# Performance work log

Hardware: AMD Instinct MI355X
Metric: run time of the kernel (lower is better)

Reference implementation:

```python
import jax, jax.numpy as jnp
import numpy as np

B, T, D_MODEL, N_HEADS = 2, 2048, 2048, 16
D_HEAD = D_MODEL // N_HEADS
SCALE = 1.0 / np.sqrt(D_HEAD)


def setup_inputs() -> dict:
    key = jax.random.key(0)
    ks = jax.random.split(key, 5)
    w_std = 1.0 / np.sqrt(D_MODEL)
    x = jax.random.normal(ks[0], (B, T, D_MODEL), dtype=jnp.float32)
    W_q = jax.random.normal(ks[1], (D_MODEL, D_MODEL), dtype=jnp.float32) * w_std
    W_k = jax.random.normal(ks[2], (D_MODEL, D_MODEL), dtype=jnp.float32) * w_std
    W_v = jax.random.normal(ks[3], (D_MODEL, D_MODEL), dtype=jnp.float32) * w_std
    W_o = jax.random.normal(ks[4], (D_MODEL, D_MODEL), dtype=jnp.float32) * w_std
    return {"x": x, "W_q": W_q, "W_k": W_k, "W_v": W_v, "W_o": W_o}


def _split_heads(y):
    # [B, T, D] -> [B, H, T, d_head]
    b, t, _ = y.shape
    return y.reshape(b, t, N_HEADS, D_HEAD).transpose(0, 2, 1, 3)


def reference(x, W_q, W_k, W_v, W_o):
    # Linear layers (torch nn.Linear: y = x @ W.T)
    Q = _split_heads(x @ W_q.T)
    K = _split_heads(x @ W_k.T)
    V = _split_heads(x @ W_v.T)
    # Causal softmax attention (math-equivalent to the tiled online-softmax loop)
    scores = jnp.einsum('bhqd,bhkd->bhqk', Q, K) * SCALE
    causal_mask = jnp.tril(jnp.ones((T, T), dtype=bool))  # [T, T]
    scores = jnp.where(causal_mask, scores, -jnp.inf)
    P = jax.nn.softmax(scores, axis=-1)
    O = jnp.einsum('bhqk,bhkd->bhqd', P, V)
    out = O.transpose(0, 2, 1, 3).reshape(B, T, D_MODEL)  # merge heads
    return out @ W_o.T
```

## Files before the change

kernel.cpp:

```cpp
#include <hip/hip_runtime.h>
#include <hip/hip_bf16.h>
#include <hip/hip_fp16.h>

#define B_   2
#define T_   2048
#define DM   2048
#define NH   16
#define DH   128
#define M_   (B_*T_)
#define SCALE_ 0.08838834764831845f

typedef _Float16 f16;
typedef f16  half8 __attribute__((ext_vector_type(8)));
typedef f16  half4 __attribute__((ext_vector_type(4)));
typedef float f32x4 __attribute__((ext_vector_type(4)));

#define GL16(gp, lp) __builtin_amdgcn_global_load_lds( \
    (const __attribute__((address_space(1))) void*)(gp), \
    (__attribute__((address_space(3))) void*)(lp), 16, 0, 0)

#define MFMA16(a, b, c) __builtin_amdgcn_mfma_f32_16x16x32_f16((a), (b), (c), 0, 0, 0)

struct CvtArgs { const float* s[5]; f16* d[5]; };

__global__ __launch_bounds__(256) void convert_all(CvtArgs a) {
    size_t i4 = (size_t)blockIdx.x * 256 + threadIdx.x;
    int r; size_t off;
    if (i4 < 2097152) { r = 0; off = i4; }
    else { size_t k = i4 - 2097152; r = 1 + (int)(k >> 20); off = k & 1048575; }
    float4 v = *((const float4*)a.s[r] + off);
    half4 h;
    h[0] = (f16)v.x; h[1] = (f16)v.y; h[2] = (f16)v.z; h[3] = (f16)v.w;
    *((half4*)a.d[r] + off) = h;
}

#define NT_K 32

__global__ __launch_bounds__(512, 2)
void qkv3(const f16* __restrict__ A, const f16* __restrict__ Bw,
          f16* __restrict__ dst)
{
    __shared__ __align__(16) char smem[114688];

    const int tid  = threadIdx.x;
    const int lane = tid & 63;
    const int w    = tid >> 6;
    const int wr   = w >> 1, wc = w & 1;

    const int id = (blockIdx.x & 7) * 64 + (blockIdx.x >> 3);
    const int bm = id & 15, bn = id >> 4;
    const int m0 = bm * 256, n0 = bn * 192;

    const int scol8 = (((tid & 7) ^ ((tid >> 3) & 7)) << 3);
    const int rc0 = (((lane >> 4) * 16)      ) ^ ((lane & 7) << 4);
    const int rc1 = (64 + (lane >> 4) * 16   ) ^ ((lane & 7) << 4);

    f32x4 acc[4][6] = {};

#define QSTAGE_A(bufb, ch, s, kt) GL16( \
    A + (size_t)(m0 + (ch)*128 + (tid>>8)*64 + (s)*32 + ((tid>>3)&31)) * 2048 + (kt)*64 + scol8, \
    smem + (bufb)*57344 + (ch)*16384 + (s)*8192 + w*1024)
#define QSTAGE_B(bufb, u, kt) GL16( \
    Bw + (size_t)(n0 + (tid>>7)*48 + (u)*16 + ((tid>>3)&15)) * 2048 + (kt)*64 + scol8, \
    smem + (bufb)*57344 + 32768 + (u)*8192 + w*1024)

    const int abase = (wr >> 1) * 16384 + (wr & 1) * 4096 + (lane & 15) * 128;
    const int bbase = 32768 + wc * 4096 + (lane & 15) * 128;

    half8 af0[4][2], af1[4][2], bnx[2];

    QSTAGE_A(0, 0, 0, 0); QSTAGE_A(0, 0, 1, 0);
    QSTAGE_A(0, 1, 0, 0); QSTAGE_A(0, 1, 1, 0);
    QSTAGE_B(0, 0, 0);    QSTAGE_B(0, 1, 0);    QSTAGE_B(0, 2, 0);
    {
        asm volatile("s_waitcnt vmcnt(2)" ::: "memory");
        __builtin_amdgcn_s_barrier();
        __builtin_amdgcn_sched_barrier(0);
        const char* buf0 = smem;
        #pragma unroll
        for (int m = 0; m < 4; ++m) {
            const char* p = buf0 + (m >> 1) * 8192 + abase + (m & 1) * 2048;
            af0[m][0] = *(const half8*)(p + rc0);
            af0[m][1] = *(const half8*)(p + rc1);
        }
        bnx[0] = *(const half8*)(buf0 + bbase + rc0);
        bnx[1] = *(const half8*)(buf0 + bbase + rc1);
    }

#define GATE(n_) do { \
    asm volatile("s_waitcnt vmcnt(" #n_ ")" ::: "memory"); \
    __builtin_amdgcn_s_barrier(); \
    __builtin_amdgcn_sched_barrier(0); \
} while (0)

#define MFC(AF, BB, f_) do { \
    __builtin_amdgcn_s_setprio(1); \
    _Pragma("unroll") \
    for (int m_ = 0; m_ < 4; ++m_) { \
        acc[m_][f_] = MFMA16(AF[m_][0], (BB)[0], acc[m_][f_]); \
        acc[m_][f_] = MFMA16(AF[m_][1], (BB)[1], acc[m_][f_]); \
    } \
    __builtin_amdgcn_s_setprio(0); \
} while (0)

#define RDB(dstv, off) do { \
    const char* p_ = buf + bbase + (off); \
    dstv[0] = *(const half8*)(p_ + rc0); \
    dstv[1] = *(const half8*)(p_ + rc1); \
} while (0)

#define BODY(t_, c_, AFC, AFN) do { \
    const char* buf  = smem + (c_) * 57344; \
    const char* nbuf = smem + ((c_) ^ 1) * 57344; \
    const int  kt    = ((t_) + 1 < NT_K) ? (t_) + 1 : (t_); \
    half8 b3[2], b1[2], b4[2], b2[2], b5[2]; \
     \
    RDB(b3, 2048); \
    QSTAGE_A((c_) ^ 1, 0, 0, kt); QSTAGE_A((c_) ^ 1, 0, 1, kt); \
    MFC(AFC, bnx, 0); \
     \
    GATE(3); \
    RDB(b1, 8192); \
    QSTAGE_A((c_) ^ 1, 1, 0, kt); QSTAGE_A((c_) ^ 1, 1, 1, kt); \
    MFC(AFC, b3, 3); \
     \
    RDB(b4, 8192 + 2048); \
    QSTAGE_B((c_) ^ 1, 0, kt); \
    MFC(AFC, b1, 1); \
     \
    GATE(5); \
    RDB(b2, 16384); \
    QSTAGE_B((c_) ^ 1, 1, kt); \
    MFC(AFC, b4, 4); \
     \
    GATE(1); \
    RDB(b5, 16384 + 2048); \
    { const char* p_ = nbuf + abase; \
      AFN[0][0] = *(const half8*)(p_ + rc0); \
      AFN[0][1] = *(const half8*)(p_ + rc1); \
      AFN[1][0] = *(const half8*)(p_ + 2048 + rc0); \
      AFN[1][1] = *(const half8*)(p_ + 2048 + rc1); } \
    QSTAGE_B((c_) ^ 1, 2, kt); \
    MFC(AFC, b2, 2); \
     \
    { const char* p_ = nbuf + 8192 + abase; \
      AFN[2][0] = *(const half8*)(p_ + rc0); \
      AFN[2][1] = *(const half8*)(p_ + rc1); \
      AFN[3][0] = *(const half8*)(p_ + 2048 + rc0); \
      AFN[3][1] = *(const half8*)(p_ + 2048 + rc1); } \
    { const char* p_ = nbuf + bbase; \
      bnx[0] = *(const half8*)(p_ + rc0); \
      bnx[1] = *(const half8*)(p_ + rc1); } \
    MFC(AFC, b5, 5); \
} while (0)

    for (int t = 0; t < NT_K; t += 2) {
        BODY(t,     0, af0, af1);
        BODY(t + 1, 1, af1, af0);
    }
#undef BODY
#undef RDB
#undef MFC
#undef GATE
#undef QSTAGE_A
#undef QSTAGE_B

    asm volatile("s_waitcnt vmcnt(0)" ::: "memory");

    #pragma unroll
    for (int m = 0; m < 4; ++m)
        #pragma unroll
        for (int f = 0; f < 6; ++f)
            #pragma unroll
            for (int j = 0; j < 4; ++j) {
                int row  = m0 + wr * 64 + m * 16 + (lane >> 4) * 4 + j;
                int gcol = n0 + wc * 96 + f * 16 + (lane & 15);
                int sec = gcol >> 11, cic = gcol & 2047;
                int b = row >> 11, tt = row & (T_ - 1);
                int h = cic >> 7, d = cic & 127;
                float cs = (sec == 0) ? SCALE_ : 1.0f;
                dst[(size_t)sec * ((size_t)M_ * 2048) +
                    ((size_t)(b * NH + h) * T_ + tt) * DH + d] = (f16)(acc[m][f][j] * cs);
            }
}

#define NT_W 32

__global__ __launch_bounds__(512, 4)
void wo2(const f16* __restrict__ A, const f16* __restrict__ Bw,
         float* __restrict__ Cf)
{
    __shared__ __align__(16) char smem[65536];

    const int tid  = threadIdx.x;
    const int lane = tid & 63;
    const int w    = tid >> 6;
    const int wr   = w >> 2, wc = w & 3;

    const int id = (blockIdx.x & 7) * 64 + (blockIdx.x >> 3);
    const int bm = id & 31, bn = id >> 5;
    const int m0 = bm * 128, n0 = bn * 128;

    const int scol8 = (((tid & 7) ^ ((tid >> 3) & 7)) << 3);
    const int rc0 = (((lane >> 4) * 16)      ) ^ ((lane & 7) << 4);
    const int rc1 = (64 + (lane >> 4) * 16   ) ^ ((lane & 7) << 4);

    f32x4 acc[4][2] = {};

#define WSTAGE_A(bufb, s, kt) GL16( \
    A + (size_t)(m0 + (tid>>8)*64 + (s)*32 + ((tid>>3)&31)) * 2048 + (kt)*64 + scol8, \
    smem + (bufb)*32768 + (s)*8192 + w*1024)
#define WSTAGE_B(bufb, u, kt) GL16( \
    Bw + (size_t)(n0 + (tid>>7)*32 + (u)*16 + ((tid>>3)&15)) * 2048 + (kt)*64 + scol8, \
    smem + (bufb)*32768 + 16384 + (u)*8192 + w*1024)

    WSTAGE_A(0, 0, 0); WSTAGE_A(0, 1, 0);
    WSTAGE_B(0, 0, 0); WSTAGE_B(0, 1, 0);

    const int abase = wr * 4096 + (lane & 15) * 128;
    const int bbase = 16384 + (wc * 16 + (lane & 15)) * 128;

    for (int t = 0; t < NT_W; ++t) {
        const int c  = t & 1;
        const char* buf = smem + c * 32768;
        const int kt = (t + 1 < NT_W) ? t + 1 : t;

        half8 af[4][2], bfr[2];
        asm volatile("s_waitcnt vmcnt(1)" ::: "memory");
        __builtin_amdgcn_s_barrier();
        __builtin_amdgcn_sched_barrier(0);
        #pragma unroll
        for (int m = 0; m < 4; ++m) {
            const char* p = buf + (m >> 1) * 8192 + abase + (m & 1) * 2048;
            af[m][0] = *(const half8*)(p + rc0);
            af[m][1] = *(const half8*)(p + rc1);
        }
        { const char* p = buf + bbase;
          bfr[0] = *(const half8*)(p + rc0); bfr[1] = *(const half8*)(p + rc1); }
        WSTAGE_A(c ^ 1, 0, kt); WSTAGE_A(c ^ 1, 1, kt);
        __builtin_amdgcn_s_setprio(1);
        #pragma unroll
        for (int m = 0; m < 4; ++m) {
            acc[m][0] = MFMA16(af[m][0], bfr[0], acc[m][0]);
            acc[m][0] = MFMA16(af[m][1], bfr[1], acc[m][0]);
        }
        __builtin_amdgcn_s_setprio(0);

        asm volatile("s_waitcnt vmcnt(2)" ::: "memory");
        __builtin_amdgcn_s_barrier();
        __builtin_amdgcn_sched_barrier(0);
        { const char* p = buf + bbase + 8192;
          bfr[0] = *(const half8*)(p + rc0); bfr[1] = *(const half8*)(p + rc1); }
        WSTAGE_B(c ^ 1, 0, kt); WSTAGE_B(c ^ 1, 1, kt);
        __builtin_amdgcn_s_setprio(1);
        #pragma unroll
        for (int m = 0; m < 4; ++m) {
            acc[m][1] = MFMA16(af[m][0], bfr[0], acc[m][1]);
            acc[m][1] = MFMA16(af[m][1], bfr[1], acc[m][1]);
        }
        __builtin_amdgcn_s_setprio(0);
        __builtin_amdgcn_s_barrier();
    }
#undef WSTAGE_A
#undef WSTAGE_B

    asm volatile("s_waitcnt vmcnt(0)" ::: "memory");

    #pragma unroll
    for (int m = 0; m < 4; ++m)
        #pragma unroll
        for (int u = 0; u < 2; ++u)
            #pragma unroll
            for (int j = 0; j < 4; ++j) {
                int row = m0 + wr * 64 + m * 16 + (lane >> 4) * 4 + j;
                int col = n0 + wc * 32 + u * 16 + (lane & 15);
                Cf[(size_t)row * 2048 + col] = acc[m][u][j];
            }
}

__global__ __launch_bounds__(256)
void vtrans(const f16* __restrict__ Vin, f16* __restrict__ Vout)
{
    __shared__ f16 ld[64][72];
    const int tid = threadIdx.x;
    const int dd = blockIdx.x;
    const int tt = blockIdx.y;
    const int bh = blockIdx.z;

    const int r  = tid >> 2;
    const int s2 = (tid & 3) * 2;

    const f16* src = Vin + ((size_t)bh * T_ + tt * 64 + r) * DH + dd * 64;
    half8 v0 = *(const half8*)(src + s2 * 8);
    half8 v1 = *(const half8*)(src + s2 * 8 + 8);
    #pragma unroll
    for (int e = 0; e < 8; ++e) ld[s2 * 8 + e][r]     = v0[e];
    #pragma unroll
    for (int e = 0; e < 8; ++e) ld[s2 * 8 + 8 + e][r] = v1[e];
    __syncthreads();

    f16* dst = Vout + ((size_t)bh * DH + dd * 64 + r) * T_ + tt * 64;
    *(half8*)(dst + s2 * 8)     = *(const half8*)&ld[r][s2 * 8];
    *(half8*)(dst + s2 * 8 + 8) = *(const half8*)&ld[r][s2 * 8 + 8];
}

#define QB 64
#define KB 64
#define PP 72
#define NQT (T_/QB)

__global__ __launch_bounds__(256, 2)
void attn_fwd(const f16* __restrict__ Q, const f16* __restrict__ K,
              const f16* __restrict__ Vt, f16* __restrict__ O)
{
    __shared__ __align__(16) char Ks[2][16384];
    __shared__ __align__(16) char Vs[2][16384];
    __shared__ __align__(16) f16 Ps[4][16][PP];

    const int tid  = threadIdx.x;
    const int lane = tid & 63;
    const int w    = tid >> 6;
    const int g    = lane >> 4;

    const int bid  = blockIdx.x;
    const int swz  = (bid & 7) * 64 + (bid >> 3);
    const int bh   = swz >> 4;
    const int pair = swz & 15;
    const size_t base = (size_t)bh * T_ * DH;
    const int b = bh >> 4, h = bh & 15;

    const int krow0 = w * 4 + g;
    const int kswz  = ((lane & 15) ^ (krow0 & 7)) << 3;
    const int vrow0 = w * 8 + (lane >> 3);
    const int vswz  = (((lane & 7) ^ ((lane >> 3) & 7)) << 3);

#define STAGE_K(c_, kv) do { \
    _Pragma("unroll") for (int i_ = 0; i_ < 4; ++i_) { \
        const f16* g_ = K + base + (size_t)((kv) + i_*16 + krow0) * DH + kswz; \
        GL16(g_, &Ks[c_][i_*4096 + w*1024]); } } while (0)
#define STAGE_V(c_, kv) do { \
    _Pragma("unroll") for (int i_ = 0; i_ < 4; ++i_) { \
        const f16* g_ = Vt + base + (size_t)(i_*32 + vrow0) * T_ + (kv) + vswz; \
        GL16(g_, &Vs[c_][i_*4096 + w*1024]); } } while (0)

#define QKT(SA, QF) do { \
    __builtin_amdgcn_s_setprio(1); \
    _Pragma("unroll") \
    for (int n_ = 0; n_ < 4; ++n_) \
        _Pragma("unroll") \
        for (int kk_ = 0; kk_ < 4; ++kk_) { \
            half8 kfv = *(const half8*)(kb + (n_*16 + (lane & 15)) * 256 + \
                ((kk_*32 + g * 8) * 2 ^ ((lane & 7) << 4))); \
            SA[n_] = MFMA16(kfv, QF[kk_], SA[n_]); \
        } \
    __builtin_amdgcn_s_setprio(0); \
} while (0)

#define SMAX(SA, MRUN, LSUM, OO) do { \
    float mx_ = SA[0][0]; \
    _Pragma("unroll") \
    for (int n_ = 0; n_ < 4; ++n_) \
        _Pragma("unroll") \
        for (int j_ = 0; j_ < 4; ++j_) mx_ = fmaxf(mx_, SA[n_][j_]); \
    mx_ = fmaxf(mx_, __shfl_xor(mx_, 16)); \
    mx_ = fmaxf(mx_, __shfl_xor(mx_, 32)); \
    if (!__all(mx_ <= MRUN + 5.f)) { \
        float mnew_ = fmaxf(MRUN, mx_); \
        float sf_ = __expf(MRUN - mnew_); \
        _Pragma("unroll") \
        for (int nn_ = 0; nn_ < 8; ++nn_) OO[nn_] *= sf_; \
        LSUM *= sf_; \
        MRUN = mnew_; \
    } \
    float rs_ = 0.f; \
    _Pragma("unroll") \
    for (int n_ = 0; n_ < 4; ++n_) \
        _Pragma("unroll") \
        for (int j_ = 0; j_ < 4; ++j_) { \
            float p_ = __expf(SA[n_][j_] - MRUN); \
            SA[n_][j_] = p_; \
            rs_ += p_; \
        } \
    LSUM += rs_; \
} while (0)

#define PFRAG(SA, BP) do { \
    _Pragma("unroll") \
    for (int n_ = 0; n_ < 4; ++n_) { \
        half4 hv_; \
        hv_[0] = (f16)SA[n_][0]; hv_[1] = (f16)SA[n_][1]; \
        hv_[2] = (f16)SA[n_][2]; hv_[3] = (f16)SA[n_][3]; \
        *reinterpret_cast<half4*>(&Ps[w][lane & 15][n_*16 + g*4]) = hv_; \
    } \
    _Pragma("unroll") \
    for (int cc_ = 0; cc_ < 2; ++cc_) \
        BP[cc_] = *reinterpret_cast<const half8*>(&Ps[w][lane & 15][cc_*32 + g*8]); \
} while (0)

#define PV(OO, BP) do { \
    __builtin_amdgcn_s_setprio(1); \
    _Pragma("unroll") \
    for (int n_ = 0; n_ < 8; ++n_) \
        _Pragma("unroll") \
        for (int cc_ = 0; cc_ < 2; ++cc_) { \
            half8 vf_ = *(const half8*)(vb + (n_*16 + (lane & 15)) * 128 + \
                ((cc_*64 + g*16) ^ ((lane & 7) << 4))); \
            OO[n_] = MFMA16(vf_, BP[cc_], OO[n_]); \
        } \
    __builtin_amdgcn_s_setprio(0); \
} while (0)

    const int qt1 = pair;
    const int qt2 = NQT - 1 - pair;
    const int nt1 = qt1 + 1;
    const int ntU = qt2 + 1;
    const int qg1 = qt1 * QB + w * 16 + (lane & 15);
    const int qg2 = qt2 * QB + w * 16 + (lane & 15);

    half8 qf1[4], qf2[4];
    #pragma unroll
    for (int kk = 0; kk < 4; ++kk) {
        qf1[kk] = *reinterpret_cast<const half8*>(
            &Q[base + (size_t)qg1 * DH + kk * 32 + g * 8]);
        qf2[kk] = *reinterpret_cast<const half8*>(
            &Q[base + (size_t)qg2 * DH + kk * 32 + g * 8]);
    }

    float mrun1 = -1e30f, lsum1 = 0.f;
    float mrun2 = -1e30f, lsum2 = 0.f;
    f32x4 o1[8] = {};
    f32x4 o2[8] = {};

    STAGE_K(0, 0);
    STAGE_V(0, 0);

    for (int it = 0; it < ntU; ++it) {
        const int c = it & 1;
        __syncthreads();
        if (it + 1 < ntU) {
            STAGE_K(c ^ 1, (it + 1) * KB);
            STAGE_V(c ^ 1, (it + 1) * KB);
        }
        const bool s1 = (it < nt1);
        const char* kb = &Ks[c][0];
        const char* vb = &Vs[c][0];

        f32x4 sa2[4] = {};
        f32x4 sa1[4] = {};

        QKT(sa2, qf2);
        if (s1) QKT(sa1, qf1);

        if (it == ntU - 1) {
            #pragma unroll
            for (int n = 0; n < 4; ++n)
                #pragma unroll
                for (int j = 0; j < 4; ++j) {
                    int kg = it * KB + n*16 + g*4 + j;
                    if (kg > qg2) sa2[n][j] = -1e30f;
                }
        }
        if (s1 && it == nt1 - 1) {
            #pragma unroll
            for (int n = 0; n < 4; ++n)
                #pragma unroll
                for (int j = 0; j < 4; ++j) {
                    int kg = it * KB + n*16 + g*4 + j;
                    if (kg > qg1) sa1[n][j] = -1e30f;
                }
        }

        SMAX(sa2, mrun2, lsum2, o2);
        half8 bp2[2];
        PFRAG(sa2, bp2);
        PV(o2, bp2);

        if (s1) {
            SMAX(sa1, mrun1, lsum1, o1);
            half8 bp1[2];
            PFRAG(sa1, bp1);
            PV(o1, bp1);
        }
    }

    {
        float l2 = lsum2;
        l2 += __shfl_xor(l2, 16);
        l2 += __shfl_xor(l2, 32);
        float invl = 1.0f / l2;
        #pragma unroll
        for (int n = 0; n < 8; ++n) {
            half4 hv;
            hv[0] = (f16)(o2[n][0] * invl); hv[1] = (f16)(o2[n][1] * invl);
            hv[2] = (f16)(o2[n][2] * invl); hv[3] = (f16)(o2[n][3] * invl);
            *reinterpret_cast<half4*>(
                &O[((size_t)(b * T_ + qg2) * NH + h) * DH + n*16 + g*4]) = hv;
        }
    }
    {
        float l1 = lsum1;
        l1 += __shfl_xor(l1, 16);
        l1 += __shfl_xor(l1, 32);
        float invl = 1.0f / l1;
        #pragma unroll
        for (int n = 0; n < 8; ++n) {
            half4 hv;
            hv[0] = (f16)(o1[n][0] * invl); hv[1] = (f16)(o1[n][1] * invl);
            hv[2] = (f16)(o1[n][2] * invl); hv[3] = (f16)(o1[n][3] * invl);
            *reinterpret_cast<half4*>(
                &O[((size_t)(b * T_ + qg1) * NH + h) * DH + n*16 + g*4]) = hv;
        }
    }
#undef PV
#undef PFRAG
#undef SMAX
#undef QKT
#undef STAGE_K
#undef STAGE_V
}

extern "C" void kernel_launch(void* const* d_in, const int* in_sizes, int n_in,
                              void* d_out, int out_size, void* d_ws, size_t ws_size,
                              hipStream_t stream)
{
    const float* x  = (const float*)d_in[0];
    const float* wq = (const float*)d_in[1];
    const float* wk = (const float*)d_in[2];
    const float* wv = (const float*)d_in[3];
    const float* wo = (const float*)d_in[4];
    float* out = (float*)d_out;

    const size_t nx = (size_t)M_ * DM;
    const size_t nw = (size_t)DM * DM;
    const size_t need = (nx * 5 + nw * 4) * sizeof(f16);
    if (ws_size < need) return;

    char* ws = (char*)d_ws;
    f16* xh  = (f16*)ws;  ws += nx * 2;
    f16* wqh = (f16*)ws;  ws += nw * 2;
    f16* wkh = (f16*)ws;  ws += nw * 2;
    f16* wvh = (f16*)ws;  ws += nw * 2;
    f16* woh = (f16*)ws;  ws += nw * 2;
    f16* Qh  = (f16*)ws;  ws += nx * 2;
    f16* Kh  = (f16*)ws;  ws += nx * 2;
    f16* Vh  = (f16*)ws;  ws += nx * 2;
    f16* Oh  = (f16*)ws;  ws += nx * 2;

    f16* Vth = xh;

    CvtArgs ca;
    ca.s[0] = x;  ca.d[0] = xh;
    ca.s[1] = wq; ca.d[1] = wqh;
    ca.s[2] = wk; ca.d[2] = wkh;
    ca.s[3] = wv; ca.d[3] = wvh;
    ca.s[4] = wo; ca.d[4] = woh;
    convert_all<<<24576, 256, 0, stream>>>(ca);

    qkv3<<<dim3(512), 512, 0, stream>>>(xh, wqh, Qh);

    vtrans<<<dim3(2, 32, 32), 256, 0, stream>>>(Vh, Vth);

    attn_fwd<<<dim3(512), 256, 0, stream>>>(Qh, Kh, Vth, Oh);

    wo2<<<dim3(512), 512, 0, stream>>>(Oh, woh, out);
}
```

Measured before the change: 232.9 us.

## Enlarge output-projection GEMM tile to 256x128 with 64x64 warp tiles

The W_o projection GEMM moves from 128x128 block tiles with 64x32 per-warp tiles to 256x128 block tiles with 64x64 per-warp tiles, launching 256 blocks instead of 512. Each warp now loads four B fragments and reuses them across four A row fragments, which raises MFMA work per LDS read and halves global reloads of the weight tiles. The staging pipeline is reorganised into two gated phases with a larger double buffer (96 KB LDS) and lower occupancy (2 blocks/SM bound). The risks are fewer blocks than compute units on the device, which causes a tail or idle units, plus extra register pressure.

```diff
diff --git a/kernel.cpp b/kernel.cpp
--- a/kernel.cpp
+++ b/kernel.cpp
@@ -186,95 +186,111 @@
 
 #define NT_W 32
 
-__global__ __launch_bounds__(512, 4)
+__global__ __launch_bounds__(512, 2)
 void wo2(const f16* __restrict__ A, const f16* __restrict__ Bw,
          float* __restrict__ Cf)
 {
-    __shared__ __align__(16) char smem[65536];
+    __shared__ __align__(16) char smem[98304];
 
     const int tid  = threadIdx.x;
     const int lane = tid & 63;
     const int w    = tid >> 6;
-    const int wr   = w >> 2, wc = w & 3;
-
-    const int id = (blockIdx.x & 7) * 64 + (blockIdx.x >> 3);
-    const int bm = id & 31, bn = id >> 5;
-    const int m0 = bm * 128, n0 = bn * 128;
+    const int wr   = w >> 1, wc = w & 1;
+
+    const int id = (blockIdx.x & 7) * 32 + (blockIdx.x >> 3);
+    const int bm = id & 15, bn = id >> 4;
+    const int m0 = bm * 256, n0 = bn * 128;
 
     const int scol8 = (((tid & 7) ^ ((tid >> 3) & 7)) << 3);
     const int rc0 = (((lane >> 4) * 16)      ) ^ ((lane & 7) << 4);
     const int rc1 = (64 + (lane >> 4) * 16   ) ^ ((lane & 7) << 4);
 
-    f32x4 acc[4][2] = {};
-
-#define WSTAGE_A(bufb, s, kt) GL16( \
-    A + (size_t)(m0 + (tid>>8)*64 + (s)*32 + ((tid>>3)&31)) * 2048 + (kt)*64 + scol8, \
-    smem + (bufb)*32768 + (s)*8192 + w*1024)
-#define WSTAGE_B(bufb, u, kt) GL16( \
-    Bw + (size_t)(n0 + (tid>>7)*32 + (u)*16 + ((tid>>3)&15)) * 2048 + (kt)*64 + scol8, \
-    smem + (bufb)*32768 + 16384 + (u)*8192 + w*1024)
-
-    WSTAGE_A(0, 0, 0); WSTAGE_A(0, 1, 0);
-    WSTAGE_B(0, 0, 0); WSTAGE_B(0, 1, 0);
-
-    const int abase = wr * 4096 + (lane & 15) * 128;
-    const int bbase = 16384 + (wc * 16 + (lane & 15)) * 128;
+    f32x4 acc[4][4] = {};
+
+#define WSA(bufb, s, kt) GL16( \
+    A + (size_t)(m0 + ((s)&1)*128 + (tid>>8)*64 + ((s)>>1)*32 + ((tid>>3)&31)) * 2048 + (kt)*64 + scol8, \
+    smem + (bufb)*49152 + (s)*8192 + w*1024)
+#define WSB(bufb, u, kt) GL16( \
+    Bw + (size_t)(n0 + (tid>>8)*64 + (u)*32 + ((tid>>3)&31)) * 2048 + (kt)*64 + scol8, \
+    smem + (bufb)*49152 + 32768 + (u)*8192 + w*1024)
+
+    WSA(0, 0, 0); WSA(0, 1, 0); WSB(0, 0, 0); WSB(0, 1, 0);
+    WSA(0, 2, 0); WSA(0, 3, 0);
+
+    const int abase = (wr >> 1) * 8192 + (wr & 1) * 4096 + (lane & 15) * 128;
+    const int bbase = 32768 + wc * 4096 + (lane & 15) * 128;
+
+#define WGATE(n_) do { \
+    asm volatile("s_waitcnt vmcnt(" #n_ ")" ::: "memory"); \
+    __builtin_amdgcn_s_barrier(); \
+    __builtin_amdgcn_sched_barrier(0); \
+} while (0)
 
     for (int t = 0; t < NT_W; ++t) {
-        const int c  = t & 1;
-        const char* buf = smem + c * 32768;
+        const int c = t & 1;
+        const char* buf = smem + c * 49152;
         const int kt = (t + 1 < NT_W) ? t + 1 : t;
 
-        half8 af[4][2], bfr[2];
-        asm volatile("s_waitcnt vmcnt(1)" ::: "memory");
-        __builtin_amdgcn_s_barrier();
-        __builtin_amdgcn_sched_barrier(0);
-        #pragma unroll
-        for (int m = 0; m < 4; ++m) {
-            const char* p = buf + (m >> 1) * 8192 + abase + (m & 1) * 2048;
+        half8 af[4][2], bf[4][2];
+
+        WGATE(2);
+        #pragma unroll
+        for (int m = 0; m < 2; ++m) {
+            const char* p = buf + abase + m * 2048;
             af[m][0] = *(const half8*)(p + rc0);
             af[m][1] = *(const half8*)(p + rc1);
         }
-        { const char* p = buf + bbase;
-          bfr[0] = *(const half8*)(p + rc0); bfr[1] = *(const half8*)(p + rc1); }
-        WSTAGE_A(c ^ 1, 0, kt); WSTAGE_A(c ^ 1, 1, kt);
+        #pragma unroll
+        for (int n = 0; n < 4; ++n) {
+            const char* p = buf + bbase + (n >> 1) * 8192 + (n & 1) * 2048;
+            bf[n][0] = *(const half8*)(p + rc0);
+            bf[n][1] = *(const half8*)(p + rc1);
+        }
+        WSA(c ^ 1, 0, kt); WSA(c ^ 1, 1, kt);
+        WSB(c ^ 1, 0, kt); WSB(c ^ 1, 1, kt);
         __builtin_amdgcn_s_setprio(1);
         #pragma unroll
-        for (int m = 0; m < 4; ++m) {
-            acc[m][0] = MFMA16(af[m][0], bfr[0], acc[m][0]);
-            acc[m][0] = MFMA16(af[m][1], bfr[1], acc[m][0]);
-        }
+        for (int m = 0; m < 2; ++m)
+            #pragma unroll
+            for (int n = 0; n < 4; ++n) {
+                acc[m][n] = MFMA16(af[m][0], bf[n][0], acc[m][n]);
+                acc[m][n] = MFMA16(af[m][1], bf[n][1], acc[m][n]);
+            }
         __builtin_amdgcn_s_setprio(0);
 
-        asm volatile("s_waitcnt vmcnt(2)" ::: "memory");
-        __builtin_amdgcn_s_barrier();
-        __builtin_amdgcn_sched_barrier(0);
-        { const char* p = buf + bbase + 8192;
-          bfr[0] = *(const half8*)(p + rc0); bfr[1] = *(const half8*)(p + rc1); }
-        WSTAGE_B(c ^ 1, 0, kt); WSTAGE_B(c ^ 1, 1, kt);
+        WGATE(4);
+        #pragma unroll
+        for (int m = 2; m < 4; ++m) {
+            const char* p = buf + 16384 + abase + (m & 1) * 2048;
+            af[m][0] = *(const half8*)(p + rc0);
+            af[m][1] = *(const half8*)(p + rc1);
+        }
+        WSA(c ^ 1, 2, kt); WSA(c ^ 1, 3, kt);
         __builtin_amdgcn_s_setprio(1);
         #pragma unroll
-        for (int m = 0; m < 4; ++m) {
-            acc[m][1] = MFMA16(af[m][0], bfr[0], acc[m][1]);
-            acc[m][1] = MFMA16(af[m][1], bfr[1], acc[m][1]);
-        }
+        for (int m = 2; m < 4; ++m)
+            #pragma unroll
+            for (int n = 0; n < 4; ++n) {
+                acc[m][n] = MFMA16(af[m][0], bf[n][0], acc[m][n]);
+                acc[m][n] = MFMA16(af[m][1], bf[n][1], acc[m][n]);
+            }
         __builtin_amdgcn_s_setprio(0);
-        __builtin_amdgcn_s_barrier();
-    }
-#undef WSTAGE_A
-#undef WSTAGE_B
+    }
+#undef WGATE
+#undef WSA
+#undef WSB
 
     asm volatile("s_waitcnt vmcnt(0)" ::: "memory");
 
     #pragma unroll
     for (int m = 0; m < 4; ++m)
         #pragma unroll
-        for (int u = 0; u < 2; ++u)
+        for (int n = 0; n < 4; ++n)
             #pragma unroll
             for (int j = 0; j < 4; ++j) {
                 int row = m0 + wr * 64 + m * 16 + (lane >> 4) * 4 + j;
-                int col = n0 + wc * 32 + u * 16 + (lane & 15);
-                Cf[(size_t)row * 2048 + col] = acc[m][u][j];
+                int col = n0 + wc * 64 + n * 16 + (lane & 15);
+                Cf[(size_t)row * 2048 + col] = acc[m][n][j];
             }
 }
 
@@ -562,5 +578,5 @@
 
     attn_fwd<<<dim3(512), 256, 0, stream>>>(Qh, Kh, Vth, Oh);
 
-    wo2<<<dim3(512), 512, 0, stream>>>(Oh, woh, out);
+    wo2<<<dim3(256), 512, 0, stream>>>(Oh, woh, out);
 }
```

New measurement: 228.4 us, median of 3. About the same (-1.9%).
